# Kernel tuning notes

Measured on AMD Instinct MI355X. Metric: run time of the kernel, lower is better.

Reference implementation:

```python
import jax, jax.numpy as jnp
import numpy as np

B, S, D, H = 1, 2048, 1024, 16
HD = D // H
DFF = 4 * D
EPS = 1e-5


def _layernorm(x, g, b):
    mu = jnp.mean(x, axis=-1, keepdims=True)
    var = jnp.mean(jnp.square(x - mu), axis=-1, keepdims=True)
    return (x - mu) * jax.lax.rsqrt(var + EPS) * g + b


def setup_inputs() -> dict:
    key = jax.random.key(0)
    ks = jax.random.split(key, 8)
    scale = 1.0 / np.sqrt(D)
    # standard ALiBi slopes: 2^(-8*i/H)
    slopes = jnp.asarray(2.0 ** (-8.0 * (np.arange(1, H + 1) / H)), dtype=jnp.float32)
    return {
        "x": jax.random.normal(ks[0], (B, S, D), jnp.float32),
        "alibi_slopes": slopes,
        "wq": jax.random.normal(ks[1], (D, D), jnp.float32) * scale,
        "wk": jax.random.normal(ks[2], (D, D), jnp.float32) * scale,
        "wv": jax.random.normal(ks[3], (D, D), jnp.float32) * scale,
        "wo": jax.random.normal(ks[4], (D, D), jnp.float32) * scale,
        "ff1_w": jax.random.normal(ks[5], (DFF, D), jnp.float32) * scale,
        "ff1_b": jnp.zeros((DFF,), jnp.float32),
        "ff2_w": jax.random.normal(ks[6], (D, DFF), jnp.float32) * (1.0 / np.sqrt(DFF)),
        "ff2_b": jnp.zeros((D,), jnp.float32),
        "ln1_g": jnp.ones((D,), jnp.float32),
        "ln1_b": jnp.zeros((D,), jnp.float32),
        "ln2_g": jnp.ones((D,), jnp.float32),
        "ln2_b": jnp.zeros((D,), jnp.float32),
    }


def reference(x, alibi_slopes, wq, wk, wv, wo, ff1_w, ff1_b, ff2_w, ff2_b,
              ln1_g, ln1_b, ln2_g, ln2_b):
    b, s, d = x.shape
    residual = x
    h = _layernorm(x, ln1_g, ln1_b)
    # projections (torch Linear: y = x @ W^T); split heads
    q = (h @ wq.T).reshape(b, s, H, HD)
    k = (h @ wk.T).reshape(b, s, H, HD)
    v = (h @ wv.T).reshape(b, s, H, HD)
    scores = jnp.einsum("bqhd,bkhd->bhqk", q, k) / np.sqrt(HD)  # [B,H,S,S]
    # ALiBi: distance[i,j] = j - i; scores -= slope * distance
    pos = jnp.arange(s, dtype=jnp.float32)
    dist = pos[None, :] - pos[:, None]                    # [S,S]
    scores = scores - alibi_slopes[None, :, None, None] * dist[None, None]
    # causal mask (query i attends to keys j <= i)
    causal = pos[:, None] >= pos[None, :]
    scores = jnp.where(causal[None, None], scores, -jnp.inf)
    attn = jax.nn.softmax(scores, axis=-1)
    out = jnp.einsum("bhqk,bkhd->bqhd", attn, v).reshape(b, s, d)
    out = out @ wo.T
    x = residual + out
    residual = x
    h2 = _layernorm(x, ln2_g, ln2_b)
    ff = jax.nn.gelu(h2 @ ff1_w.T + ff1_b, approximate=False) @ ff2_w.T + ff2_b
    return residual + ff
```

## Files before the change

kernel.cpp:

```cpp
#include <hip/hip_runtime.h>
#include <math.h>

typedef unsigned short u16;
typedef __bf16 bf16x8 __attribute__((ext_vector_type(8)));
typedef float f32x4 __attribute__((ext_vector_type(4)));
typedef u16 u16x4 __attribute__((ext_vector_type(4)));
typedef u16 u16x8 __attribute__((ext_vector_type(8)));

#define DEV __device__ __forceinline__

DEV u16 f2bf(float f) {
  unsigned u = __builtin_bit_cast(unsigned, f);
  u += 0x7FFFu + ((u >> 16) & 1u);
  return (u16)(u >> 16);
}
DEV float bf2f(u16 b) {
  unsigned u = ((unsigned)b) << 16;
  return __builtin_bit_cast(float, u);
}

DEV void gload16(const void* g, void* l) {
  __builtin_amdgcn_global_load_lds((__attribute__((address_space(1))) void*)g,
                                   (__attribute__((address_space(3))) void*)l, 16, 0, 0);
}

__launch_bounds__(256)
__global__ void cvt_all(const float* __restrict__ wq, const float* __restrict__ wk,
                        const float* __restrict__ wv, const float* __restrict__ wo,
                        const float* __restrict__ f1, const float* __restrict__ f2,
                        u16* __restrict__ dq, u16* __restrict__ dk, u16* __restrict__ dv,
                        u16* __restrict__ dwo, u16* __restrict__ df1, u16* __restrict__ df2) {
  int i = blockIdx.x * 256 + threadIdx.x;
  const float* src;
  u16* dst;
  int local;
  if (i < (1 << 18)) { src = wq; dst = dq; local = i; }
  else if (i < (2 << 18)) { src = wk; dst = dk; local = i - (1 << 18); }
  else if (i < (3 << 18)) { src = wv; dst = dv; local = i - (2 << 18); }
  else if (i < (4 << 18)) { src = wo; dst = dwo; local = i - (3 << 18); }
  else if (i < (4 << 18) + (1 << 20)) { src = f1; dst = df1; local = i - (4 << 18); }
  else { src = f2; dst = df2; local = i - ((4 << 18) + (1 << 20)); }
  float4 v = ((const float4*)src)[local];
  u16x4 o = { f2bf(v.x), f2bf(v.y), f2bf(v.z), f2bf(v.w) };
  ((u16x4*)dst)[local] = o;
}

__launch_bounds__(256)
__global__ void ln_rows(const float* __restrict__ x, const float* __restrict__ gam,
                        const float* __restrict__ bet, u16* __restrict__ out) {
  int row = blockIdx.x;
  int t = threadIdx.x;
  float4 v = ((const float4*)(x + (size_t)row * 1024))[t];
  float s = v.x + v.y + v.z + v.w;
  float s2 = v.x * v.x + v.y * v.y + v.z * v.z + v.w * v.w;
  for (int off = 1; off < 64; off <<= 1) {
    s += __shfl_xor(s, off);
    s2 += __shfl_xor(s2, off);
  }
  __shared__ float red[8];
  int wv = t >> 6, ln = t & 63;
  if (ln == 0) { red[wv] = s; red[wv + 4] = s2; }
  __syncthreads();
  s = red[0] + red[1] + red[2] + red[3];
  s2 = red[4] + red[5] + red[6] + red[7];
  float mu = s * (1.f / 1024.f);
  float var = s2 * (1.f / 1024.f) - mu * mu;
  float rs = rsqrtf(var + 1e-5f);
  float4 gv = ((const float4*)gam)[t];
  float4 bv = ((const float4*)bet)[t];
  u16x4 o = { f2bf((v.x - mu) * rs * gv.x + bv.x), f2bf((v.y - mu) * rs * gv.y + bv.y),
              f2bf((v.z - mu) * rs * gv.z + bv.z), f2bf((v.w - mu) * rs * gv.w + bv.w) };
  ((u16x4*)(out + (size_t)row * 1024))[t] = o;
}

__launch_bounds__(256)
__global__ void ln2_add(const float* __restrict__ x, const float* __restrict__ P0,
                        const float* __restrict__ P1, const float* __restrict__ gam,
                        const float* __restrict__ bet, float* __restrict__ x2,
                        u16* __restrict__ out) {
  int row = blockIdx.x;
  int t = threadIdx.x;
  size_t base = (size_t)row * 256 + t;
  float4 xv = ((const float4*)x)[base];
  float4 p0 = ((const float4*)P0)[base];
  float4 p1 = ((const float4*)P1)[base];
  float4 v = { xv.x + p0.x + p1.x, xv.y + p0.y + p1.y,
               xv.z + p0.z + p1.z, xv.w + p0.w + p1.w };
  ((float4*)x2)[base] = v;
  float s = v.x + v.y + v.z + v.w;
  float s2 = v.x * v.x + v.y * v.y + v.z * v.z + v.w * v.w;
  for (int off = 1; off < 64; off <<= 1) {
    s += __shfl_xor(s, off);
    s2 += __shfl_xor(s2, off);
  }
  __shared__ float red[8];
  int wv = t >> 6, ln = t & 63;
  if (ln == 0) { red[wv] = s; red[wv + 4] = s2; }
  __syncthreads();
  s = red[0] + red[1] + red[2] + red[3];
  s2 = red[4] + red[5] + red[6] + red[7];
  float mu = s * (1.f / 1024.f);
  float var = s2 * (1.f / 1024.f) - mu * mu;
  float rs = rsqrtf(var + 1e-5f);
  float4 gv = ((const float4*)gam)[t];
  float4 bv = ((const float4*)bet)[t];
  u16x4 o = { f2bf((v.x - mu) * rs * gv.x + bv.x), f2bf((v.y - mu) * rs * gv.y + bv.y),
              f2bf((v.z - mu) * rs * gv.z + bv.z), f2bf((v.w - mu) * rs * gv.w + bv.w) };
  ((u16x4*)(out + (size_t)row * 1024))[t] = o;
}

__launch_bounds__(256)
__global__ void final_add(const float* __restrict__ x2, const float* __restrict__ b2,
                          const u16* __restrict__ Q0, const u16* __restrict__ Q1,
                          float* __restrict__ out) {
  int row = blockIdx.x;
  int t = threadIdx.x;
  size_t base = (size_t)row * 256 + t;
  float4 xv = ((const float4*)x2)[base];
  float4 bv = ((const float4*)b2)[t];
  u16x4 q0 = ((const u16x4*)Q0)[base];
  u16x4 q1 = ((const u16x4*)Q1)[base];
  float4 o = { xv.x + bv.x + bf2f(q0[0]) + bf2f(q1[0]),
               xv.y + bv.y + bf2f(q0[1]) + bf2f(q1[1]),
               xv.z + bv.z + bf2f(q0[2]) + bf2f(q1[2]),
               xv.w + bv.w + bf2f(q0[3]) + bf2f(q1[3]) };
  ((float4*)out)[base] = o;
}

__launch_bounds__(256)
__global__ void transpose_v(const u16* __restrict__ V, u16* __restrict__ Vt) {
  const int st = blockIdx.x, h = blockIdx.y;
  __shared__ u16 tile[64][72];
  const int t = threadIdx.x;
  const int r = t >> 3, c8 = t & 7;
#pragma unroll
  for (int i = 0; i < 2; ++i) {
    int row = i * 32 + r;
    *(u16x8*)&tile[row][c8 * 8] =
        *(const u16x8*)&V[(size_t)(st * 64 + row) * 1024 + h * 64 + c8 * 8];
  }
  __syncthreads();
#pragma unroll
  for (int i = 0; i < 2; ++i) {
    int d = i * 32 + r;
    u16x8 o;
#pragma unroll
    for (int jj = 0; jj < 8; ++jj) o[jj] = tile[c8 * 8 + jj][d];
    *(u16x8*)&Vt[(size_t)(h * 64 + d) * 2048 + st * 64 + c8 * 8] = o;
  }
}

template <int BM, int BN, int WR, int WC, int EPI, int SPLITK>
__launch_bounds__(256, 2)
__global__ void gemm_bt(const u16* __restrict__ A, const u16* __restrict__ B,
                        void* __restrict__ C, const float* __restrict__ bias,
                        const float* __restrict__ resid, int M, int N, int K,
                        size_t zoff) {
  constexpr int FM = BM / WR / 16;
  constexpr int FN = BN / WC / 16;
  __shared__ u16 As[BM * 32];
  __shared__ u16 Bs[BN * 32];
  const int t = threadIdx.x, lane = t & 63, w = t >> 6;
  const int wr = w / WC, wc = w % WC;
  const int g = lane >> 4, l16 = lane & 15;
  const int m0 = blockIdx.y * BM, n0 = blockIdx.x * BN;
  const int ks = K / SPLITK;
  const int k0 = (SPLITK > 1) ? blockIdx.z * ks : 0;
  const size_t cbase = (SPLITK > 1) ? (size_t)blockIdx.z * zoff : 0;
  f32x4 acc[FM][FN] = {};
  const int nkt = ks >> 5;
  for (int kt = 0; kt < nkt; ++kt) {
    const u16* Ag = A + (size_t)m0 * K + k0 + kt * 32;
    const u16* Bg = B + (size_t)n0 * K + k0 + kt * 32;
#pragma unroll
    for (int i = 0; i < BM / 64; ++i) {
      int c = i * 256 + t;
      gload16(Ag + (size_t)(c >> 2) * K + (c & 3) * 8, &As[(i * 256 + w * 64) * 8]);
    }
#pragma unroll
    for (int i = 0; i < BN / 64; ++i) {
      int c = i * 256 + t;
      gload16(Bg + (size_t)(c >> 2) * K + (c & 3) * 8, &Bs[(i * 256 + w * 64) * 8]);
    }
    __syncthreads();
    bf16x8 af[FM], bfr[FN];
#pragma unroll
    for (int m = 0; m < FM; ++m)
      af[m] = *(const bf16x8*)&As[(wr * FM * 16 + m * 16 + l16) * 32 + g * 8];
#pragma unroll
    for (int n = 0; n < FN; ++n)
      bfr[n] = *(const bf16x8*)&Bs[(wc * FN * 16 + n * 16 + l16) * 32 + g * 8];
#pragma unroll
    for (int m = 0; m < FM; ++m)
#pragma unroll
      for (int n = 0; n < FN; ++n)
        acc[m][n] = __builtin_amdgcn_mfma_f32_16x16x32_bf16(af[m], bfr[n], acc[m][n], 0, 0, 0);
    __syncthreads();
  }
#pragma unroll
  for (int m = 0; m < FM; ++m)
#pragma unroll
    for (int n = 0; n < FN; ++n)
#pragma unroll
      for (int r = 0; r < 4; ++r) {
        int row = m0 + wr * FM * 16 + m * 16 + g * 4 + r;
        int col = n0 + wc * FN * 16 + n * 16 + l16;
        size_t idx = (size_t)row * N + col;
        float v = acc[m][n][r];
        if constexpr (EPI == 0) {
          ((u16*)C)[cbase + idx] = f2bf(v);
        } else if constexpr (EPI == 1) {
          v += bias[col];
          v = 0.5f * v * (1.f + erff(v * 0.70710678118f));
          ((u16*)C)[idx] = f2bf(v);
        } else if constexpr (EPI == 2) {
          ((float*)C)[idx] = v + bias[col] + resid[idx];
        } else if constexpr (EPI == 3) {
          ((float*)C)[idx] = v + resid[idx];
        } else {
          ((float*)C)[cbase + idx] = v;
        }
      }
}

__launch_bounds__(256, 2)
__global__ void gemm_qkv64(const u16* __restrict__ A, const u16* __restrict__ B0,
                           const u16* __restrict__ B1, const u16* __restrict__ B2,
                           u16* __restrict__ C0, u16* __restrict__ C1, u16* __restrict__ C2) {
  constexpr int FM = 4, FN = 2;
  const int K = 1024, N = 1024;
  const int which = blockIdx.x >> 3;
  const u16* B = which == 0 ? B0 : which == 1 ? B1 : B2;
  u16* C = which == 0 ? C0 : which == 1 ? C1 : C2;
  __shared__ u16 As[64 * 32];
  __shared__ u16 Bs[128 * 32];
  const int t = threadIdx.x, lane = t & 63, w = t >> 6;
  const int wc = w;
  const int g = lane >> 4, l16 = lane & 15;
  const int m0 = blockIdx.y * 64, n0 = (blockIdx.x & 7) * 128;
  f32x4 acc[FM][FN] = {};
  for (int kt = 0; kt < 32; ++kt) {
    const u16* Ag = A + (size_t)m0 * K + kt * 32;
    const u16* Bg = B + (size_t)n0 * K + kt * 32;
    {
      int c = t;
      gload16(Ag + (size_t)(c >> 2) * K + (c & 3) * 8, &As[(w * 64) * 8]);
    }
#pragma unroll
    for (int i = 0; i < 2; ++i) {
      int c = i * 256 + t;
      gload16(Bg + (size_t)(c >> 2) * K + (c & 3) * 8, &Bs[(i * 256 + w * 64) * 8]);
    }
    __syncthreads();
    bf16x8 af[FM], bfr[FN];
#pragma unroll
    for (int m = 0; m < FM; ++m)
      af[m] = *(const bf16x8*)&As[(m * 16 + l16) * 32 + g * 8];
#pragma unroll
    for (int n = 0; n < FN; ++n)
      bfr[n] = *(const bf16x8*)&Bs[(wc * FN * 16 + n * 16 + l16) * 32 + g * 8];
#pragma unroll
    for (int m = 0; m < FM; ++m)
#pragma unroll
      for (int n = 0; n < FN; ++n)
        acc[m][n] = __builtin_amdgcn_mfma_f32_16x16x32_bf16(af[m], bfr[n], acc[m][n], 0, 0, 0);
    __syncthreads();
  }
#pragma unroll
  for (int m = 0; m < FM; ++m)
#pragma unroll
    for (int n = 0; n < FN; ++n)
#pragma unroll
      for (int r = 0; r < 4; ++r) {
        int row = m0 + m * 16 + g * 4 + r;
        int col = n0 + wc * FN * 16 + n * 16 + l16;
        C[(size_t)row * N + col] = f2bf(acc[m][n][r]);
      }
}

__launch_bounds__(256, 2)
__global__ void attn_fwd(const u16* __restrict__ Q, const u16* __restrict__ Kb,
                         const u16* __restrict__ Vt, const float* __restrict__ slopes,
                         u16* __restrict__ O) {
  const int bx = blockIdx.x;
  const int h = blockIdx.y;
  const int t = threadIdx.x, lane = t & 63, w = t >> 6;
  const int g = lane >> 4, l16 = lane & 15;
  const float slope = slopes[h];

  __shared__ u16 Ks[2][4096];
  __shared__ u16 Vs[2][4096];
  __shared__ u16 Ps[4][16][72];

  const int r0 = w * 8 + (lane >> 3), r1 = 32 + r0;
  const int c8 = lane & 7;
  const int c0s = c8 ^ (r0 & 7), c1s = c8 ^ (r1 & 7);
  const int sw = l16 & 7;

#pragma unroll 1
  for (int pi = 0; pi < 2; ++pi) {
    const int qb = pi == 0 ? bx : 31 - bx;
    const int q0 = qb * 64 + w * 16;

    bf16x8 qf[2];
#pragma unroll
    for (int kk = 0; kk < 2; ++kk)
      qf[kk] = *(const bf16x8*)&Q[(size_t)(q0 + l16) * 1024 + h * 64 + kk * 32 + g * 8];

    f32x4 o_acc[4] = {};
    float m_run[4], l_run[4];
#pragma unroll
    for (int r = 0; r < 4; ++r) { m_run[r] = -1e30f; l_run[r] = 0.f; }

    __syncthreads();
    gload16(Kb + (size_t)(0 + r0) * 1024 + h * 64 + c0s * 8, &Ks[0][(w * 64) * 8]);
    gload16(Kb + (size_t)(0 + r1) * 1024 + h * 64 + c1s * 8, &Ks[0][(256 + w * 64) * 8]);
    gload16(Vt + (size_t)(h * 64 + r0) * 2048 + 0 + c0s * 8, &Vs[0][(w * 64) * 8]);
    gload16(Vt + (size_t)(h * 64 + r1) * 2048 + 0 + c1s * 8, &Vs[0][(256 + w * 64) * 8]);
    __syncthreads();

    int cur = 0;
    for (int j = 0; j <= qb; ++j) {
      const int kv0 = j * 64;
      if (j < qb) {
        const int nv0 = kv0 + 64;
        gload16(Kb + (size_t)(nv0 + r0) * 1024 + h * 64 + c0s * 8, &Ks[cur ^ 1][(w * 64) * 8]);
        gload16(Kb + (size_t)(nv0 + r1) * 1024 + h * 64 + c1s * 8, &Ks[cur ^ 1][(256 + w * 64) * 8]);
        gload16(Vt + (size_t)(h * 64 + r0) * 2048 + nv0 + c0s * 8, &Vs[cur ^ 1][(w * 64) * 8]);
        gload16(Vt + (size_t)(h * 64 + r1) * 2048 + nv0 + c1s * 8, &Vs[cur ^ 1][(256 + w * 64) * 8]);
      }
      f32x4 s[4];
#pragma unroll
      for (int n = 0; n < 4; ++n) {
        bf16x8 kf0 = *(const bf16x8*)&Ks[cur][(n * 16 + l16) * 64 + ((g ^ sw) * 8)];
        bf16x8 kf1 = *(const bf16x8*)&Ks[cur][(n * 16 + l16) * 64 + (((4 + g) ^ sw) * 8)];
        f32x4 z = {};
        s[n] = __builtin_amdgcn_mfma_f32_16x16x32_bf16(qf[0], kf0, z, 0, 0, 0);
        s[n] = __builtin_amdgcn_mfma_f32_16x16x32_bf16(qf[1], kf1, s[n], 0, 0, 0);
      }
      float sv[4][4];
      float mtile[4] = { -1e30f, -1e30f, -1e30f, -1e30f };
#pragma unroll
      for (int n = 0; n < 4; ++n) {
        int kj = kv0 + n * 16 + l16;
#pragma unroll
        for (int r = 0; r < 4; ++r) {
          int qi = q0 + g * 4 + r;
          float val = s[n][r] * 0.125f - slope * (float)(kj - qi);
          val = (kj <= qi) ? val : -1e30f;
          sv[n][r] = val;
          mtile[r] = fmaxf(mtile[r], val);
        }
      }
#pragma unroll
      for (int r = 0; r < 4; ++r) {
        float v = mtile[r];
        v = fmaxf(v, __shfl_xor(v, 1));
        v = fmaxf(v, __shfl_xor(v, 2));
        v = fmaxf(v, __shfl_xor(v, 4));
        v = fmaxf(v, __shfl_xor(v, 8));
        mtile[r] = v;
      }
      float sc[4];
#pragma unroll
      for (int r = 0; r < 4; ++r) {
        float mnew = fmaxf(m_run[r], mtile[r]);
        sc[r] = __expf(m_run[r] - mnew);
        m_run[r] = mnew;
      }
      float tsum[4] = { 0.f, 0.f, 0.f, 0.f };
#pragma unroll
      for (int n = 0; n < 4; ++n)
#pragma unroll
        for (int r = 0; r < 4; ++r) {
          float p = __expf(sv[n][r] - m_run[r]);
          sv[n][r] = p;
          tsum[r] += p;
        }
#pragma unroll
      for (int r = 0; r < 4; ++r) {
        float v = tsum[r];
        v += __shfl_xor(v, 1);
        v += __shfl_xor(v, 2);
        v += __shfl_xor(v, 4);
        v += __shfl_xor(v, 8);
        l_run[r] = l_run[r] * sc[r] + v;
      }
#pragma unroll
      for (int d = 0; d < 4; ++d)
#pragma unroll
        for (int r = 0; r < 4; ++r) o_acc[d][r] *= sc[r];
#pragma unroll
      for (int n = 0; n < 4; ++n)
#pragma unroll
        for (int r = 0; r < 4; ++r)
          Ps[w][g * 4 + r][n * 16 + l16] = f2bf(sv[n][r]);
      bf16x8 pf[2];
#pragma unroll
      for (int kk = 0; kk < 2; ++kk)
        pf[kk] = *(const bf16x8*)&Ps[w][l16][kk * 32 + g * 8];
#pragma unroll
      for (int d = 0; d < 4; ++d) {
#pragma unroll
        for (int kk = 0; kk < 2; ++kk) {
          bf16x8 vv = *(const bf16x8*)&Vs[cur][(d * 16 + l16) * 64 + (((kk * 4 + g) ^ sw) * 8)];
          o_acc[d] = __builtin_amdgcn_mfma_f32_16x16x32_bf16(pf[kk], vv, o_acc[d], 0, 0, 0);
        }
      }
      __syncthreads();
      cur ^= 1;
    }
#pragma unroll
    for (int d = 0; d < 4; ++d)
#pragma unroll
      for (int r = 0; r < 4; ++r) {
        int row = q0 + g * 4 + r;
        O[(size_t)row * 1024 + h * 64 + d * 16 + l16] = f2bf(o_acc[d][r] / l_run[r]);
      }
  }
}

extern "C" void kernel_launch(void* const* d_in, const int* in_sizes, int n_in,
                              void* d_out, int out_size, void* d_ws, size_t ws_size,
                              hipStream_t stream) {
  const float* x = (const float*)d_in[0];
  const float* slopes = (const float*)d_in[1];
  const float* wq = (const float*)d_in[2];
  const float* wk = (const float*)d_in[3];
  const float* wv = (const float*)d_in[4];
  const float* wo = (const float*)d_in[5];
  const float* ff1w = (const float*)d_in[6];
  const float* ff1b = (const float*)d_in[7];
  const float* ff2w = (const float*)d_in[8];
  const float* ff2b = (const float*)d_in[9];
  const float* ln1g = (const float*)d_in[10];
  const float* ln1b = (const float*)d_in[11];
  const float* ln2g = (const float*)d_in[12];
  const float* ln2b = (const float*)d_in[13];
  float* out = (float*)d_out;

  if (ws_size < (size_t)(56u << 20)) return;

  char* ws = (char*)d_ws;
  u16* hbuf = (u16*)(ws + 0);
  u16* Qb = (u16*)(ws + (4u << 20));
  u16* Kbf = (u16*)(ws + (8u << 20));
  u16* Vbf = (u16*)(ws + (12u << 20));
  u16* Vtb = (u16*)(ws + (16u << 20));
  float* P0 = (float*)(ws + (4u << 20));
  float* P1 = (float*)(ws + (12u << 20));
  u16* ffact = Qb;
  float* x2 = (float*)(ws + (20u << 20));
  u16* h2 = (u16*)(ws + (28u << 20));
  u16* Q1p = h2;
  u16* wqb = (u16*)(ws + (32u << 20));
  u16* wkb = (u16*)(ws + (34u << 20));
  u16* wvb = (u16*)(ws + (36u << 20));
  u16* wob = (u16*)(ws + (38u << 20));
  u16* ff1wb = (u16*)(ws + (40u << 20));
  u16* ff2wb = (u16*)(ws + (48u << 20));
  u16* attnO = hbuf;
  u16* Q0p = hbuf;
  const size_t q1off = (size_t)(28u << 20) / 2;

  cvt_all<<<12288, 256, 0, stream>>>(wq, wk, wv, wo, ff1w, ff2w,
                                     wqb, wkb, wvb, wob, ff1wb, ff2wb);

  ln_rows<<<2048, 256, 0, stream>>>(x, ln1g, ln1b, hbuf);
  gemm_qkv64<<<dim3(24, 32), 256, 0, stream>>>(hbuf, wqb, wkb, wvb, Qb, Kbf, Vbf);
  transpose_v<<<dim3(32, 16), 256, 0, stream>>>(Vbf, Vtb);
  attn_fwd<<<dim3(16, 16), 256, 0, stream>>>(Qb, Kbf, Vtb, slopes, attnO);
  gemm_bt<64, 128, 1, 4, 4, 2><<<dim3(8, 32, 2), 256, 0, stream>>>(
      attnO, wob, P0, nullptr, nullptr, 2048, 1024, 1024, (size_t)2048 * 1024);
  ln2_add<<<2048, 256, 0, stream>>>(x, P0, P1, ln2g, ln2b, x2, h2);
  gemm_bt<128, 128, 2, 2, 1, 1><<<dim3(32, 16), 256, 0, stream>>>(
      h2, ff1wb, ffact, ff1b, nullptr, 2048, 4096, 1024, 0);
  gemm_bt<64, 128, 1, 4, 0, 2><<<dim3(8, 32, 2), 256, 0, stream>>>(
      ffact, ff2wb, Q0p, nullptr, nullptr, 2048, 1024, 4096, q1off);
  final_add<<<2048, 256, 0, stream>>>(x2, ff2b, Q0p, Q1p, out);
}
```

Baseline: 206.7 us.

## Split attention KV work across two wave groups with split-K softmax merge

The attention kernel now launches 512 threads per block as two groups of four waves. Each block handles a pair of query tiles, 33 KV tiles in total, and the groups split these evenly: group 0 finishes the short query tile and starts the long one, and group 1 handles the rest of the long tile. The two partial softmax states for the long tile are merged through shared memory using the running max and sum. This halves the serial KV loop per block at the cost of more shared memory, one occupancy slot per CU, and a final merge pass. s_setprio hints are also added around the MFMA sections.

```diff
diff --git a/kernel.cpp b/kernel.cpp
--- a/kernel.cpp
+++ b/kernel.cpp
@@ -278,66 +278,91 @@
       }
 }
 
-__launch_bounds__(256, 2)
+__launch_bounds__(512, 1)
 __global__ void attn_fwd(const u16* __restrict__ Q, const u16* __restrict__ Kb,
                          const u16* __restrict__ Vt, const float* __restrict__ slopes,
                          u16* __restrict__ O) {
   const int bx = blockIdx.x;
   const int h = blockIdx.y;
-  const int t = threadIdx.x, lane = t & 63, w = t >> 6;
+  const int t = threadIdx.x, lane = t & 63, w8 = t >> 6;
+  const int grp = w8 >> 2, w = w8 & 3;
   const int g = lane >> 4, l16 = lane & 15;
   const float slope = slopes[h];
-
-  __shared__ u16 Ks[2][4096];
-  __shared__ u16 Vs[2][4096];
-  __shared__ u16 Ps[4][16][72];
+  const int TA = bx + 1;
+  const int qbB = 31 - bx;
+
+  __shared__ u16 Ks[2][2][4096];
+  __shared__ u16 Vs[2][2][4096];
+  __shared__ u16 Ps[8][16][72];
+  __shared__ float Bo[2][64][68];
+  __shared__ float Bm[2][64], Bl[2][64];
 
   const int r0 = w * 8 + (lane >> 3), r1 = 32 + r0;
   const int c8 = lane & 7;
   const int c0s = c8 ^ (r0 & 7), c1s = c8 ^ (r1 & 7);
   const int sw = l16 & 7;
 
-#pragma unroll 1
-  for (int pi = 0; pi < 2; ++pi) {
-    const int qb = pi == 0 ? bx : 31 - bx;
-    const int q0 = qb * 64 + w * 16;
-
-    bf16x8 qf[2];
-#pragma unroll
-    for (int kk = 0; kk < 2; ++kk)
-      qf[kk] = *(const bf16x8*)&Q[(size_t)(q0 + l16) * 1024 + h * 64 + kk * 32 + g * 8];
-
-    f32x4 o_acc[4] = {};
-    float m_run[4], l_run[4];
-#pragma unroll
-    for (int r = 0; r < 4; ++r) { m_run[r] = -1e30f; l_run[r] = 0.f; }
-
-    __syncthreads();
-    gload16(Kb + (size_t)(0 + r0) * 1024 + h * 64 + c0s * 8, &Ks[0][(w * 64) * 8]);
-    gload16(Kb + (size_t)(0 + r1) * 1024 + h * 64 + c1s * 8, &Ks[0][(256 + w * 64) * 8]);
-    gload16(Vt + (size_t)(h * 64 + r0) * 2048 + 0 + c0s * 8, &Vs[0][(w * 64) * 8]);
-    gload16(Vt + (size_t)(h * 64 + r1) * 2048 + 0 + c1s * 8, &Vs[0][(256 + w * 64) * 8]);
-    __syncthreads();
-
-    int cur = 0;
-    for (int j = 0; j <= qb; ++j) {
-      const int kv0 = j * 64;
-      if (j < qb) {
-        const int nv0 = kv0 + 64;
-        gload16(Kb + (size_t)(nv0 + r0) * 1024 + h * 64 + c0s * 8, &Ks[cur ^ 1][(w * 64) * 8]);
-        gload16(Kb + (size_t)(nv0 + r1) * 1024 + h * 64 + c1s * 8, &Ks[cur ^ 1][(256 + w * 64) * 8]);
-        gload16(Vt + (size_t)(h * 64 + r0) * 2048 + nv0 + c0s * 8, &Vs[cur ^ 1][(w * 64) * 8]);
-        gload16(Vt + (size_t)(h * 64 + r1) * 2048 + nv0 + c1s * 8, &Vs[cur ^ 1][(256 + w * 64) * 8]);
-      }
+  auto stage = [&](int buf, int kv0) {
+    gload16(Kb + (size_t)(kv0 + r0) * 1024 + h * 64 + c0s * 8, &Ks[grp][buf][(w * 64) * 8]);
+    gload16(Kb + (size_t)(kv0 + r1) * 1024 + h * 64 + c1s * 8, &Ks[grp][buf][(256 + w * 64) * 8]);
+    gload16(Vt + (size_t)(h * 64 + r0) * 2048 + kv0 + c0s * 8, &Vs[grp][buf][(w * 64) * 8]);
+    gload16(Vt + (size_t)(h * 64 + r1) * 2048 + kv0 + c1s * 8, &Vs[grp][buf][(256 + w * 64) * 8]);
+  };
+  auto kvOf = [&](int idx) { return idx < TA ? idx * 64 : (idx - TA) * 64; };
+
+  const int myStart = grp * 17;
+  const int myEnd = grp == 0 ? 17 : 33;
+
+  int qb = grp == 0 ? bx : qbB;
+  int q0 = qb * 64 + w * 16;
+  bf16x8 qf[2];
+#pragma unroll
+  for (int kk = 0; kk < 2; ++kk)
+    qf[kk] = *(const bf16x8*)&Q[(size_t)(q0 + l16) * 1024 + h * 64 + kk * 32 + g * 8];
+  f32x4 o_acc[4] = {};
+  float m_run[4], l_run[4];
+#pragma unroll
+  for (int r = 0; r < 4; ++r) { m_run[r] = -1e30f; l_run[r] = 0.f; }
+
+  stage(0, kvOf(myStart));
+  __syncthreads();
+
+  int cur = 0;
+  for (int it = 0; it < 17; ++it) {
+    const int idx = myStart + it;
+    const bool active = idx < myEnd;
+    if (grp == 0 && idx == TA) {
+#pragma unroll
+      for (int d = 0; d < 4; ++d)
+#pragma unroll
+        for (int r = 0; r < 4; ++r) {
+          int row = q0 + g * 4 + r;
+          O[(size_t)row * 1024 + h * 64 + d * 16 + l16] = f2bf(o_acc[d][r] / l_run[r]);
+        }
+      qb = qbB;
+      q0 = qb * 64 + w * 16;
+#pragma unroll
+      for (int kk = 0; kk < 2; ++kk)
+        qf[kk] = *(const bf16x8*)&Q[(size_t)(q0 + l16) * 1024 + h * 64 + kk * 32 + g * 8];
+#pragma unroll
+      for (int d = 0; d < 4; ++d) o_acc[d] = f32x4{};
+#pragma unroll
+      for (int r = 0; r < 4; ++r) { m_run[r] = -1e30f; l_run[r] = 0.f; }
+    }
+    if (idx + 1 < myEnd) stage(cur ^ 1, kvOf(idx + 1));
+    if (active) {
+      const int kv0 = kvOf(idx);
       f32x4 s[4];
+      __builtin_amdgcn_s_setprio(1);
 #pragma unroll
       for (int n = 0; n < 4; ++n) {
-        bf16x8 kf0 = *(const bf16x8*)&Ks[cur][(n * 16 + l16) * 64 + ((g ^ sw) * 8)];
-        bf16x8 kf1 = *(const bf16x8*)&Ks[cur][(n * 16 + l16) * 64 + (((4 + g) ^ sw) * 8)];
+        bf16x8 kf0 = *(const bf16x8*)&Ks[grp][cur][(n * 16 + l16) * 64 + ((g ^ sw) * 8)];
+        bf16x8 kf1 = *(const bf16x8*)&Ks[grp][cur][(n * 16 + l16) * 64 + (((4 + g) ^ sw) * 8)];
         f32x4 z = {};
         s[n] = __builtin_amdgcn_mfma_f32_16x16x32_bf16(qf[0], kf0, z, 0, 0, 0);
         s[n] = __builtin_amdgcn_mfma_f32_16x16x32_bf16(qf[1], kf1, s[n], 0, 0, 0);
       }
+      __builtin_amdgcn_s_setprio(0);
       float sv[4][4];
       float mtile[4] = { -1e30f, -1e30f, -1e30f, -1e30f };
 #pragma unroll
@@ -394,29 +419,54 @@
       for (int n = 0; n < 4; ++n)
 #pragma unroll
         for (int r = 0; r < 4; ++r)
-          Ps[w][g * 4 + r][n * 16 + l16] = f2bf(sv[n][r]);
+          Ps[w8][g * 4 + r][n * 16 + l16] = f2bf(sv[n][r]);
       bf16x8 pf[2];
 #pragma unroll
       for (int kk = 0; kk < 2; ++kk)
-        pf[kk] = *(const bf16x8*)&Ps[w][l16][kk * 32 + g * 8];
+        pf[kk] = *(const bf16x8*)&Ps[w8][l16][kk * 32 + g * 8];
+      __builtin_amdgcn_s_setprio(1);
 #pragma unroll
       for (int d = 0; d < 4; ++d) {
 #pragma unroll
         for (int kk = 0; kk < 2; ++kk) {
-          bf16x8 vv = *(const bf16x8*)&Vs[cur][(d * 16 + l16) * 64 + (((kk * 4 + g) ^ sw) * 8)];
+          bf16x8 vv = *(const bf16x8*)&Vs[grp][cur][(d * 16 + l16) * 64 + (((kk * 4 + g) ^ sw) * 8)];
           o_acc[d] = __builtin_amdgcn_mfma_f32_16x16x32_bf16(pf[kk], vv, o_acc[d], 0, 0, 0);
         }
       }
-      __syncthreads();
-      cur ^= 1;
-    }
-#pragma unroll
-    for (int d = 0; d < 4; ++d)
-#pragma unroll
-      for (int r = 0; r < 4; ++r) {
-        int row = q0 + g * 4 + r;
-        O[(size_t)row * 1024 + h * 64 + d * 16 + l16] = f2bf(o_acc[d][r] / l_run[r]);
-      }
+      __builtin_amdgcn_s_setprio(0);
+    }
+    __syncthreads();
+    cur ^= 1;
+  }
+#pragma unroll
+  for (int d = 0; d < 4; ++d)
+#pragma unroll
+    for (int r = 0; r < 4; ++r)
+      Bo[grp][w * 16 + g * 4 + r][d * 16 + l16] = o_acc[d][r];
+  if (l16 == 0) {
+#pragma unroll
+    for (int r = 0; r < 4; ++r) {
+      Bm[grp][w * 16 + g * 4 + r] = m_run[r];
+      Bl[grp][w * 16 + g * 4 + r] = l_run[r];
+    }
+  }
+  __syncthreads();
+  if (grp == 0) {
+#pragma unroll
+    for (int rr = 0; rr < 4; ++rr) {
+      const int row = w * 16 + g * 4 + rr;
+      float m0 = Bm[0][row], m1 = Bm[1][row];
+      float mm = fmaxf(m0, m1);
+      float w0 = __expf(m0 - mm), w1 = __expf(m1 - mm);
+      float ll = Bl[0][row] * w0 + Bl[1][row] * w1;
+      float inv = 1.f / ll;
+#pragma unroll
+      for (int d = 0; d < 4; ++d) {
+        int col = d * 16 + l16;
+        float o = Bo[0][row][col] * w0 + Bo[1][row][col] * w1;
+        O[(size_t)(qbB * 64 + row) * 1024 + h * 64 + col] = f2bf(o * inv);
+      }
+    }
   }
 }
 
@@ -469,7 +519,7 @@
   ln_rows<<<2048, 256, 0, stream>>>(x, ln1g, ln1b, hbuf);
   gemm_qkv64<<<dim3(24, 32), 256, 0, stream>>>(hbuf, wqb, wkb, wvb, Qb, Kbf, Vbf);
   transpose_v<<<dim3(32, 16), 256, 0, stream>>>(Vbf, Vtb);
-  attn_fwd<<<dim3(16, 16), 256, 0, stream>>>(Qb, Kbf, Vtb, slopes, attnO);
+  attn_fwd<<<dim3(16, 16), 512, 0, stream>>>(Qb, Kbf, Vtb, slopes, attnO);
   gemm_bt<64, 128, 1, 4, 4, 2><<<dim3(8, 32, 2), 256, 0, stream>>>(
       attnO, wob, P0, nullptr, nullptr, 2048, 1024, 1024, (size_t)2048 * 1024);
   ln2_add<<<2048, 256, 0, stream>>>(x, P0, P1, ln2g, ln2b, x2, h2);
```

Measured after the change: 192.2 us. -7.0%, faster.
